# Optimization experiments

Hardware: AMD Instinct MI355X
Metric: run time of the kernel (lower is better)

## Reference

```python
import jax, jax.numpy as jnp
import numpy as np

CH = 64          # channels per plane
GS = 256         # base grid size
N_PTS = 500_000  # query points
BOUND = 1.0
A = -0.75        # torch bicubic coefficient


def _avg_pool(p):
    # torch F.avg_pool2d(kernel=3, stride=2, padding=1, count_include_pad=True) on (C,H,W)
    s = jax.lax.reduce_window(p, 0.0, jax.lax.add, (1, 3, 3), (1, 2, 2),
                              [(0, 0), (1, 1), (1, 1)])
    return s / 9.0


def _cubic_w(t):
    # Keys cubic conv weights (a=-0.75) for taps at offsets [-1,0,1,2]; t in [0,1). -> (4, M)
    def k1(x):  # |x| <= 1
        return ((A + 2.0) * x - (A + 3.0)) * x * x + 1.0
    def k2(x):  # 1 < |x| < 2
        return ((A * x - 5.0 * A) * x + 8.0 * A) * x - 4.0 * A
    return jnp.stack([k2(t + 1.0), k1(t), k1(1.0 - t), k2(2.0 - t)])


def _sample_plane(plane, gx, gy):
    # bicubic grid_sample, padding_mode='border', align_corners=True
    # plane: (C,H,W); gx,gy: (M,) grid coords in [-1,1] convention. -> (M,C)
    C, H, W = plane.shape
    x = (gx + 1.0) * 0.5 * (W - 1)  # unnormalize (align_corners=True)
    y = (gy + 1.0) * 0.5 * (H - 1)
    x0 = jnp.floor(x)
    y0 = jnp.floor(y)
    wx = _cubic_w(x - x0)  # (4,M)
    wy = _cubic_w(y - y0)  # (4,M)
    offs = jnp.arange(-1, 3, dtype=jnp.int32)[:, None]
    ix = jnp.clip(x0.astype(jnp.int32)[None, :] + offs, 0, W - 1)  # (4,M) border clamp
    iy = jnp.clip(y0.astype(jnp.int32)[None, :] + offs, 0, H - 1)
    out = jnp.zeros((C, x.shape[0]), plane.dtype)
    for j in range(4):
        row = wx[0] * plane[:, iy[j], ix[0]]
        for i in range(1, 4):
            row = row + wx[i] * plane[:, iy[j], ix[i]]  # (C,M) gather + fma
        out = out + wy[j] * row
    return out.T  # (M,C)


def setup_inputs() -> dict:
    key = jax.random.key(0)
    kc, kx, ky, kz = jax.random.split(key, 4)
    coordinates = jax.random.uniform(kc, (N_PTS, 3), jnp.float32, -1.0, 1.0)
    px0 = jax.random.normal(kx, (CH, GS, GS), jnp.float32) * 0.001
    py0 = jax.random.normal(ky, (CH, GS, GS), jnp.float32) * 0.001
    pz0 = jax.random.normal(kz, (CH, GS, GS), jnp.float32) * 0.001
    px1, py1, pz1 = _avg_pool(px0), _avg_pool(py0), _avg_pool(pz0)
    px2, py2, pz2 = _avg_pool(px1), _avg_pool(py1), _avg_pool(pz1)
    return dict(coordinates=coordinates, px0=px0, py0=py0, pz0=pz0,
                px1=px1, py1=py1, pz1=pz1, px2=px2, py2=py2, pz2=pz2)


def reference(coordinates, px0, py0, pz0, px1, py1, pz1, px2, py2, pz2):
    # Faithful to torch: coords mapped to [0,1] and fed to grid_sample as-is
    c = (coordinates + BOUND) / (2.0 * BOUND)  # (N,3), lives in [0,1] of the [-1,1] grid space
    feats = []
    for pxy, pyz, pxz in ((px0, py0, pz0), (px1, py1, pz1), (px2, py2, pz2)):
        f = (_sample_plane(pxy, c[:, 0], c[:, 1])
             + _sample_plane(pyz, c[:, 1], c[:, 2])
             + _sample_plane(pxz, c[:, 0], c[:, 2]))
        feats.append(f)
    return jnp.concatenate(feats, axis=-1)  # (N, 3*CH)
```

## Files before the change

kernel.cpp:

```cpp
#include <hip/hip_runtime.h>
#include <hip/hip_fp16.h>

#define NPTS 500000
#define NBINS 32768
#define NSUPER 8192

#define PLANE_SCALE 1024.0f
#define INV_PLANE_SCALE 0.0009765625f

__device__ __forceinline__ void cubic_w(float t, float w[4]) {
  const float a = -0.75f;
  const float t1 = t + 1.0f;
  w[0] = ((a * t1 - 5.0f * a) * t1 + 8.0f * a) * t1 - 4.0f * a;
  w[1] = ((a + 2.0f) * t - (a + 3.0f)) * t * t + 1.0f;
  const float u = 1.0f - t;
  w[2] = ((a + 2.0f) * u - (a + 3.0f)) * u * u + 1.0f;
  const float t2 = 2.0f - t;
  w[3] = ((a * t2 - 5.0f * a) * t2 + 8.0f * a) * t2 - 4.0f * a;
}

__global__ __launch_bounds__(256) void transpose_chw_hwc_f16(
    const float* __restrict__ p0, const float* __restrict__ p1,
    const float* __restrict__ p2, __half* __restrict__ dst, int HW) {
  __shared__ float lds[64][65];
  const float* src = (blockIdx.y == 0) ? p0 : ((blockIdx.y == 1) ? p1 : p2);
  __half* out = dst + (size_t)blockIdx.y * (size_t)HW * 64;
  const int pixBase = blockIdx.x * 64;
  const int tid = threadIdx.x;
  const int lane = tid & 63;
  const int quad = tid >> 6;
#pragma unroll
  for (int k = 0; k < 16; ++k) {
    const int c = k * 4 + quad;
    lds[c][lane] = src[(size_t)c * HW + pixBase + lane];
  }
  __syncthreads();
#pragma unroll
  for (int k = 0; k < 16; ++k) {
    const int pp = k * 4 + quad;
    out[(size_t)(pixBase + pp) * 64 + lane] =
        __float2half(lds[lane][pp] * PLANE_SCALE);
  }
}

__device__ __forceinline__ unsigned spread3(unsigned v) {
  return (v & 1u) | ((v & 2u) << 2) | ((v & 4u) << 4) | ((v & 8u) << 6) |
         ((v & 16u) << 8);
}

__device__ __forceinline__ unsigned compact3(unsigned v) {
  return (v & 1u) | ((v >> 2) & 2u) | ((v >> 4) & 4u) | ((v >> 6) & 8u) |
         ((v >> 8) & 16u);
}

__device__ __forceinline__ int bin_of(float cx, float cy, float cz) {
  int xq = (int)((cx + 1.0f) * 16.0f);
  int yq = (int)((cy + 1.0f) * 16.0f);
  int zq = (int)((cz + 1.0f) * 16.0f);
  xq = xq < 0 ? 0 : (xq > 31 ? 31 : xq);
  yq = yq < 0 ? 0 : (yq > 31 ? 31 : yq);
  zq = zq < 0 ? 0 : (zq > 31 ? 31 : zq);
  return (int)(spread3((unsigned)xq) | (spread3((unsigned)yq) << 1) |
               (spread3((unsigned)zq) << 2));
}

__global__ __launch_bounds__(256) void bin_count(
    const float* __restrict__ coords, int* __restrict__ counts) {
  const int pt = blockIdx.x * 256 + threadIdx.x;
  if (pt >= NPTS) return;
  const int b = bin_of(coords[pt * 3], coords[pt * 3 + 1], coords[pt * 3 + 2]);
  atomicAdd(&counts[b], 1);
}

__global__ __launch_bounds__(1024) void bin_scan(
    const int* __restrict__ counts, int* __restrict__ cursor) {
  __shared__ int lds[1024];
  const int t = threadIdx.x;
  const int base = t * 32;
  int s = 0;
#pragma unroll
  for (int i = 0; i < 32; ++i) s += counts[base + i];
  lds[t] = s;
  __syncthreads();
  int own = s;
  for (int off = 1; off < 1024; off <<= 1) {
    int v = (t >= off) ? lds[t - off] : 0;
    __syncthreads();
    lds[t] += v;
    __syncthreads();
  }
  int run = lds[t] - own;
#pragma unroll
  for (int i = 0; i < 32; ++i) {
    cursor[base + i] = run;
    run += counts[base + i];
  }
}

__global__ __launch_bounds__(256) void bin_scatter_prep(
    const float* __restrict__ coords, int* __restrict__ cursor,
    uint4* __restrict__ wrec) {
  const int pt = blockIdx.x * 256 + threadIdx.x;
  if (pt >= NPTS) return;
  const float x = coords[pt * 3], y = coords[pt * 3 + 1],
              z = coords[pt * 3 + 2];
  const int b = bin_of(x, y, z);
  const int pos = atomicAdd(&cursor[b], 1);

  const int qx0 = ((int)compact3((unsigned)b)) & ~1;
  const int qy0 = ((int)compact3((unsigned)b >> 1)) & ~1;
  const int qz = (int)compact3((unsigned)b >> 2);
  const float vin[3] = {x, y, z};

#pragma unroll
  for (int s = 0; s < 3; ++s) {
    const int W = (s == 0) ? 256 : ((s == 1) ? 128 : 64);
    const float hw = 0.5f * (float)(W - 1);
    const int fb[3] = {(int)floorf((1.0f + (float)qx0 * 0.03125f) * hw),
                       (int)floorf((1.0f + (float)qy0 * 0.03125f) * hw),
                       (int)floorf((1.0f + (float)qz * 0.03125f) * hw)};
    uint wp[6];
    int rel[3];
#pragma unroll
    for (int a = 0; a < 3; ++a) {
      const float c = (vin[a] + 1.0f) * 0.5f;
      const float gx = (c + 1.0f) * 0.5f * (float)(W - 1);
      const float x0f = floorf(gx);
      float w[4];
      cubic_w(gx - x0f, w);
      int r = (int)x0f - fb[a];
      const int rmax = (a == 2) ? 4 : 12;
      r = r < 0 ? 0 : (r > rmax ? rmax : r);
      rel[a] = r;
      const __half2 lo = __halves2half2(__float2half(w[0]), __float2half(w[1]));
      const __half2 hi = __halves2half2(__float2half(w[2]), __float2half(w[3]));
      wp[a * 2] = *(const uint*)&lo;
      wp[a * 2 + 1] = *(const uint*)&hi;
    }
    uint4* dst = wrec + ((size_t)s * NPTS + pos) * 2;
    dst[0] = make_uint4(wp[0], wp[1], wp[2], wp[3]);
    dst[1] = make_uint4(
        wp[4], wp[5],
        (uint)(rel[0] * 4) | ((uint)(rel[1] * 4) << 8) | ((uint)rel[2] << 16),
        (uint)pt);
  }
}

__global__ __launch_bounds__(256, 4) void sample_super(
    const uint4* __restrict__ wrec, const ushort* __restrict__ tp,
    const int* __restrict__ endc, float* __restrict__ out) {
  __shared__ uint4 win[2048];

  const int orig = blockIdx.x;
  const int sb = (orig & 7) * (NSUPER / 8) + (orig >> 3);
  const int b0 = sb * 4;
  const int start = (b0 == 0) ? 0 : endc[b0 - 1];
  const int end = endc[b0 + 3];
  if (start >= end) return;

  const int s = blockIdx.y;
  const int h = blockIdx.z;
  const int W = (s == 0) ? 256 : ((s == 1) ? 128 : 64);
  const size_t sbase = (s == 0) ? 0 : ((s == 1) ? 12582912 : 15728640);
  const size_t psz = (size_t)W * W * 64;
  const float hw = 0.5f * (float)(W - 1);

  const int qx0 = ((int)compact3((unsigned)b0)) & ~1;
  const int qy0 = ((int)compact3((unsigned)b0 >> 1)) & ~1;
  const int qz = (int)compact3((unsigned)b0 >> 2);
  const int wbx = (int)floorf((1.0f + (float)qx0 * 0.03125f) * hw) - 1;
  const int wby = (int)floorf((1.0f + (float)qy0 * 0.03125f) * hw) - 1;
  const int wbz = (int)floorf((1.0f + (float)qz * 0.03125f) * hw) - 1;

  const char* tpb = (const char*)(tp + sbase) + h * 64;
  const int tid = threadIdx.x;
  const int wave = tid >> 6;
  const int lane = tid & 63;
  const int px = lane >> 2;
  const int cgl = lane & 3;
#pragma unroll
  for (int k = 0; k < 8; ++k) {
    const int row = k * 4 + wave;
    int p, grow, cb;
    if (row < 16) {
      p = 0;
      grow = wby + row;
      cb = wbx;
    } else if (row < 24) {
      p = 1;
      grow = wbz + row - 16;
      cb = wby;
    } else {
      p = 2;
      grow = wbz + row - 24;
      cb = wbx;
    }
    grow = grow < 0 ? 0 : (grow > W - 1 ? W - 1 : grow);
    int gcol = cb + px;
    gcol = gcol < 0 ? 0 : (gcol > W - 1 ? W - 1 : gcol);
    const char* src = tpb + (size_t)p * psz * 2 +
                      ((size_t)grow * W + gcol) * 128 + cgl * 16;
#if __has_builtin(__builtin_amdgcn_global_load_lds)
    __builtin_amdgcn_global_load_lds((const uint*)src,
                                     (uint*)&win[row * 64], 16, 0, 0);
#else
    win[row * 64 + lane] = *reinterpret_cast<const uint4*>(src);
#endif
  }
  __syncthreads();

  const int lanegrp = tid >> 3;
  const int i8 = tid & 7;
  const int cg = tid & 3;
  const int colpair = (tid >> 2) & 1;

  for (int i0 = start; i0 < end; i0 += 32) {
    const int slot = i0 + lanegrp;
    if (slot >= end) break;
    const uint4 r0 = wrec[((size_t)s * NPTS + slot) * 2];
    const uint4 r1 = wrec[((size_t)s * NPTS + slot) * 2 + 1];
    const int pt = (int)r1.w;
    const int relx4 = (int)(r1.z & 255u);
    const int rely4 = (int)((r1.z >> 8) & 255u);
    const int relz = (int)((r1.z >> 16) & 255u);
    const int rely = rely4 >> 2;

    const __half2 hx01 = *(const __half2*)&r0.x;
    const __half2 hx23 = *(const __half2*)&r0.y;
    const __half2 hy01 = *(const __half2*)&r0.z;
    const __half2 hy23 = *(const __half2*)&r0.w;
    const __half2 hz01 = *(const __half2*)&r1.x;
    const __half2 hz23 = *(const __half2*)&r1.y;
    __half2 wyb[4], wzb[4];
    wyb[0] = __half2half2(__low2half(hy01));
    wyb[1] = __half2half2(__high2half(hy01));
    wyb[2] = __half2half2(__low2half(hy23));
    wyb[3] = __half2half2(__high2half(hy23));
    wzb[0] = __half2half2(__low2half(hz01));
    wzb[1] = __half2half2(__high2half(hz01));
    wzb[2] = __half2half2(__low2half(hz23));
    wzb[3] = __half2half2(__high2half(hz23));
    const __half2 cxA =
        __half2half2(colpair ? __high2half(hx01) : __low2half(hx01));
    const __half2 cxB =
        __half2half2(colpair ? __high2half(hx23) : __low2half(hx23));
    const __half2 cyA =
        __half2half2(colpair ? __high2half(hy01) : __low2half(hy01));
    const __half2 cyB =
        __half2half2(colpair ? __high2half(hy23) : __low2half(hy23));

    const int bXY = rely * 64 + relx4 + i8;
    const int bYZ = 1024 + relz * 64 + rely4 + i8;
    const int bXZ = 1536 + relz * 64 + relx4 + i8;

    __half2 acc0 = __float2half2_rn(0.0f), acc1 = acc0, acc2 = acc0,
            acc3 = acc0;

#define PLANE(BASE, CWA, CWB, RW)                                   \
  _Pragma("unroll") for (int j = 0; j < 4; ++j) {                   \
    const __half2 mA = __hmul2(CWA, RW[j]);                         \
    const __half2 mB = __hmul2(CWB, RW[j]);                         \
    const uint4 vA = win[(BASE) + j * 64];                          \
    const uint4 vB = win[(BASE) + j * 64 + 8];                      \
    acc0 = __hfma2(mA, *(const __half2*)&vA.x, acc0);               \
    acc1 = __hfma2(mA, *(const __half2*)&vA.y, acc1);               \
    acc2 = __hfma2(mA, *(const __half2*)&vA.z, acc2);               \
    acc3 = __hfma2(mA, *(const __half2*)&vA.w, acc3);               \
    acc0 = __hfma2(mB, *(const __half2*)&vB.x, acc0);               \
    acc1 = __hfma2(mB, *(const __half2*)&vB.y, acc1);               \
    acc2 = __hfma2(mB, *(const __half2*)&vB.z, acc2);               \
    acc3 = __hfma2(mB, *(const __half2*)&vB.w, acc3);               \
  }

    PLANE(bXY, cxA, cxB, wyb);
    PLANE(bYZ, cyA, cyB, wzb);
    PLANE(bXZ, cxA, cxB, wzb);
#undef PLANE

    {
      uint u0 = *(const uint*)&acc0, u1 = *(const uint*)&acc1,
           u2 = *(const uint*)&acc2, u3 = *(const uint*)&acc3;
      const uint p0 = __shfl_xor((int)u0, 4, 64);
      const uint p1 = __shfl_xor((int)u1, 4, 64);
      const uint p2 = __shfl_xor((int)u2, 4, 64);
      const uint p3 = __shfl_xor((int)u3, 4, 64);
      acc0 = __hadd2(acc0, *(const __half2*)&p0);
      acc1 = __hadd2(acc1, *(const __half2*)&p1);
      acc2 = __hadd2(acc2, *(const __half2*)&p2);
      acc3 = __hadd2(acc3, *(const __half2*)&p3);
    }

    const __half2 o0 = colpair ? acc2 : acc0;
    const __half2 o1 = colpair ? acc3 : acc1;
    const float2 f0 = __half22float2(o0);
    const float2 f1 = __half22float2(o1);
    *reinterpret_cast<float4*>(out + (size_t)pt * 192 + s * 64 + h * 32 +
                               cg * 8 + colpair * 4) =
        make_float4(f0.x * INV_PLANE_SCALE, f0.y * INV_PLANE_SCALE,
                    f1.x * INV_PLANE_SCALE, f1.y * INV_PLANE_SCALE);
  }
}

__device__ __forceinline__ void sample_acc_chw(const float* __restrict__ plane,
                                               int W, float gx, float gy,
                                               int cg, float4& acc) {
  const float x = (gx + 1.0f) * 0.5f * (float)(W - 1);
  const float y = (gy + 1.0f) * 0.5f * (float)(W - 1);
  const float x0f = floorf(x), y0f = floorf(y);
  float wx[4], wy[4];
  cubic_w(x - x0f, wx);
  cubic_w(y - y0f, wy);
  const int x0 = (int)x0f, y0 = (int)y0f;
  int ix[4], iy[4];
#pragma unroll
  for (int i = 0; i < 4; ++i) {
    int xi = x0 - 1 + i;
    ix[i] = xi < 0 ? 0 : (xi > W - 1 ? W - 1 : xi);
    int yi = y0 - 1 + i;
    iy[i] = yi < 0 ? 0 : (yi > W - 1 ? W - 1 : yi);
  }
  const size_t HW = (size_t)W * W;
  float r[4] = {acc.x, acc.y, acc.z, acc.w};
#pragma unroll
  for (int cc = 0; cc < 4; ++cc) {
    const float* pc = plane + (size_t)(cg * 4 + cc) * HW;
    float a = 0.f;
#pragma unroll
    for (int j = 0; j < 4; ++j) {
      const float* rb = pc + (size_t)iy[j] * W;
      float row = 0.f;
#pragma unroll
      for (int i = 0; i < 4; ++i) row += wx[i] * rb[ix[i]];
      a += wy[j] * row;
    }
    r[cc] += a;
  }
  acc = make_float4(r[0], r[1], r[2], r[3]);
}

__global__ __launch_bounds__(256) void sample_fallback(
    const float* __restrict__ coords, const float* __restrict__ px0,
    const float* __restrict__ py0, const float* __restrict__ pz0,
    const float* __restrict__ px1, const float* __restrict__ py1,
    const float* __restrict__ pz1, const float* __restrict__ px2,
    const float* __restrict__ py2, const float* __restrict__ pz2,
    float* __restrict__ out) {
  const int t = blockIdx.x * 256 + threadIdx.x;
  const int pt = t >> 4;
  const int cg = t & 15;
  if (pt >= NPTS) return;
  const float cx = (coords[pt * 3 + 0] + 1.0f) * 0.5f;
  const float cy = (coords[pt * 3 + 1] + 1.0f) * 0.5f;
  const float cz = (coords[pt * 3 + 2] + 1.0f) * 0.5f;
  const float* xs[3] = {px0, px1, px2};
  const float* ys[3] = {py0, py1, py2};
  const float* zs[3] = {pz0, pz1, pz2};
  const int sw[3] = {256, 128, 64};
  float* optr = out + (size_t)pt * 192 + cg * 4;
#pragma unroll
  for (int s = 0; s < 3; ++s) {
    const int W = sw[s];
    float4 acc = make_float4(0.f, 0.f, 0.f, 0.f);
    sample_acc_chw(xs[s], W, cx, cy, cg, acc);
    sample_acc_chw(ys[s], W, cy, cz, cg, acc);
    sample_acc_chw(zs[s], W, cx, cz, cg, acc);
    *reinterpret_cast<float4*>(optr + s * 64) = acc;
  }
}

extern "C" void kernel_launch(void* const* d_in, const int* in_sizes, int n_in,
                              void* d_out, int out_size, void* d_ws,
                              size_t ws_size, hipStream_t stream) {
  const float* coords = (const float*)d_in[0];
  const float* px0 = (const float*)d_in[1];
  const float* py0 = (const float*)d_in[2];
  const float* pz0 = (const float*)d_in[3];
  const float* px1 = (const float*)d_in[4];
  const float* py1 = (const float*)d_in[5];
  const float* pz1 = (const float*)d_in[6];
  const float* px2 = (const float*)d_in[7];
  const float* py2 = (const float*)d_in[8];
  const float* pz2 = (const float*)d_in[9];
  float* out = (float*)d_out;

  const size_t TP_BYTES = 33030144;
  const size_t CNT_OFF = TP_BYTES;
  const size_t CUR_OFF = CNT_OFF + 131072;
  const size_t REC_OFF = CUR_OFF + 131072;
  const size_t NEEDED = REC_OFF + (size_t)NPTS * 3 * 32;

  if (ws_size >= NEEDED) {
    __half* tp = (__half*)d_ws;
    int* counts = (int*)((char*)d_ws + CNT_OFF);
    int* cursor = (int*)((char*)d_ws + CUR_OFF);
    uint4* wrec = (uint4*)((char*)d_ws + REC_OFF);

    transpose_chw_hwc_f16<<<dim3(65536 / 64, 3), 256, 0, stream>>>(
        px0, py0, pz0, tp + 0, 65536);
    transpose_chw_hwc_f16<<<dim3(16384 / 64, 3), 256, 0, stream>>>(
        px1, py1, pz1, tp + 12582912, 16384);
    transpose_chw_hwc_f16<<<dim3(4096 / 64, 3), 256, 0, stream>>>(
        px2, py2, pz2, tp + 15728640, 4096);

    hipMemsetAsync(counts, 0, NBINS * sizeof(int), stream);
    const int pblocks = (NPTS + 255) / 256;
    bin_count<<<pblocks, 256, 0, stream>>>(coords, counts);
    bin_scan<<<1, 1024, 0, stream>>>(counts, cursor);
    bin_scatter_prep<<<pblocks, 256, 0, stream>>>(coords, cursor, wrec);

    sample_super<<<dim3(NSUPER, 3, 2), 256, 0, stream>>>(
        wrec, (const ushort*)tp, cursor, out);
  } else {
    const int sample_blocks = (NPTS * 16 + 255) / 256;
    sample_fallback<<<sample_blocks, 256, 0, stream>>>(
        coords, px0, py0, pz0, px1, py1, pz1, px2, py2, pz2, out);
  }
}
```

Baseline: 322.9 us.

## Use per-scale superbin sizes with a smaller LDS window

The superbin grouping now depends on scale. The finest scale groups 4 bins with a 12x16 window, and the coarser scales group 16 bins, so fewer blocks each reuse a loaded plane window over more points. The LDS window shrinks from 2048 to 1792 entries (rows 16/8/8 become 12/8/8), and launch bounds go from 4 to 5 blocks per CU to raise occupancy. The relative offsets and clamp limits in prep are changed to match the new window shapes. In exchange, the grid still launches 8192 blocks for every scale, and those beyond the superbin count for scales 1 and 2 exit immediately.

```diff
diff --git a/kernel.cpp b/kernel.cpp
--- a/kernel.cpp
+++ b/kernel.cpp
@@ -3,7 +3,6 @@
 
 #define NPTS 500000
 #define NBINS 32768
-#define NSUPER 8192
 
 #define PLANE_SCALE 1024.0f
 #define INV_PLANE_SCALE 0.0009765625f
@@ -107,18 +106,17 @@
   const int b = bin_of(x, y, z);
   const int pos = atomicAdd(&cursor[b], 1);
 
-  const int qx0 = ((int)compact3((unsigned)b)) & ~1;
-  const int qy0 = ((int)compact3((unsigned)b >> 1)) & ~1;
-  const int qz = (int)compact3((unsigned)b >> 2);
   const float vin[3] = {x, y, z};
 
 #pragma unroll
   for (int s = 0; s < 3; ++s) {
     const int W = (s == 0) ? 256 : ((s == 1) ? 128 : 64);
     const float hw = 0.5f * (float)(W - 1);
-    const int fb[3] = {(int)floorf((1.0f + (float)qx0 * 0.03125f) * hw),
-                       (int)floorf((1.0f + (float)qy0 * 0.03125f) * hw),
-                       (int)floorf((1.0f + (float)qz * 0.03125f) * hw)};
+    const int msk = (s == 0) ? 3 : 15;
+    const int bm = b & ~msk;
+    const int q0[3] = {(int)compact3((unsigned)bm),
+                       (int)compact3((unsigned)bm >> 1),
+                       (int)compact3((unsigned)bm >> 2)};
     uint wp[6];
     int rel[3];
 #pragma unroll
@@ -128,8 +126,9 @@
       const float x0f = floorf(gx);
       float w[4];
       cubic_w(gx - x0f, w);
-      int r = (int)x0f - fb[a];
-      const int rmax = (a == 2) ? 4 : 12;
+      const int fb = (int)floorf((1.0f + (float)q0[a] * 0.03125f) * hw);
+      int r = (int)x0f - fb;
+      const int rmax = (a == 0) ? 12 : ((a == 1) ? 8 : 4);
       r = r < 0 ? 0 : (r > rmax ? rmax : r);
       rel[a] = r;
       const __half2 lo = __halves2half2(__float2half(w[0]), __float2half(w[1]));
@@ -146,31 +145,34 @@
   }
 }
 
-__global__ __launch_bounds__(256, 4) void sample_super(
+__global__ __launch_bounds__(256, 5) void sample_super(
     const uint4* __restrict__ wrec, const ushort* __restrict__ tp,
     const int* __restrict__ endc, float* __restrict__ out) {
-  __shared__ uint4 win[2048];
-
+  __shared__ uint4 win[1792];
+
+  const int s = blockIdx.y;
+  const int NSUP = (s == 0) ? 8192 : 2048;
+  const int m = (s == 0) ? 4 : 16;
   const int orig = blockIdx.x;
-  const int sb = (orig & 7) * (NSUPER / 8) + (orig >> 3);
-  const int b0 = sb * 4;
+  if (orig >= NSUP) return;
+  const int sb = (orig & 7) * (NSUP / 8) + (orig >> 3);
+  const int b0 = sb * m;
   const int start = (b0 == 0) ? 0 : endc[b0 - 1];
-  const int end = endc[b0 + 3];
+  const int end = endc[b0 + m - 1];
   if (start >= end) return;
 
-  const int s = blockIdx.y;
   const int h = blockIdx.z;
   const int W = (s == 0) ? 256 : ((s == 1) ? 128 : 64);
   const size_t sbase = (s == 0) ? 0 : ((s == 1) ? 12582912 : 15728640);
   const size_t psz = (size_t)W * W * 64;
   const float hw = 0.5f * (float)(W - 1);
 
-  const int qx0 = ((int)compact3((unsigned)b0)) & ~1;
-  const int qy0 = ((int)compact3((unsigned)b0 >> 1)) & ~1;
-  const int qz = (int)compact3((unsigned)b0 >> 2);
+  const int qx0 = (int)compact3((unsigned)b0);
+  const int qy0 = (int)compact3((unsigned)b0 >> 1);
+  const int qz0 = (int)compact3((unsigned)b0 >> 2);
   const int wbx = (int)floorf((1.0f + (float)qx0 * 0.03125f) * hw) - 1;
   const int wby = (int)floorf((1.0f + (float)qy0 * 0.03125f) * hw) - 1;
-  const int wbz = (int)floorf((1.0f + (float)qz * 0.03125f) * hw) - 1;
+  const int wbz = (int)floorf((1.0f + (float)qz0 * 0.03125f) * hw) - 1;
 
   const char* tpb = (const char*)(tp + sbase) + h * 64;
   const int tid = threadIdx.x;
@@ -179,20 +181,20 @@
   const int px = lane >> 2;
   const int cgl = lane & 3;
 #pragma unroll
-  for (int k = 0; k < 8; ++k) {
+  for (int k = 0; k < 7; ++k) {
     const int row = k * 4 + wave;
     int p, grow, cb;
-    if (row < 16) {
+    if (row < 12) {
       p = 0;
       grow = wby + row;
       cb = wbx;
-    } else if (row < 24) {
+    } else if (row < 20) {
       p = 1;
-      grow = wbz + row - 16;
+      grow = wbz + row - 12;
       cb = wby;
     } else {
       p = 2;
-      grow = wbz + row - 24;
+      grow = wbz + row - 20;
       cb = wbx;
     }
     grow = grow < 0 ? 0 : (grow > W - 1 ? W - 1 : grow);
@@ -250,8 +252,8 @@
         __half2half2(colpair ? __high2half(hy23) : __low2half(hy23));
 
     const int bXY = rely * 64 + relx4 + i8;
-    const int bYZ = 1024 + relz * 64 + rely4 + i8;
-    const int bXZ = 1536 + relz * 64 + relx4 + i8;
+    const int bYZ = 768 + relz * 64 + rely4 + i8;
+    const int bXZ = 1280 + relz * 64 + relx4 + i8;
 
     __half2 acc0 = __float2half2_rn(0.0f), acc1 = acc0, acc2 = acc0,
             acc3 = acc0;
@@ -408,7 +410,7 @@
     bin_scan<<<1, 1024, 0, stream>>>(counts, cursor);
     bin_scatter_prep<<<pblocks, 256, 0, stream>>>(coords, cursor, wrec);
 
-    sample_super<<<dim3(NSUPER, 3, 2), 256, 0, stream>>>(
+    sample_super<<<dim3(8192, 3, 2), 256, 0, stream>>>(
         wrec, (const ushort*)tp, cursor, out);
   } else {
     const int sample_blocks = (NPTS * 16 + 255) / 256;
```

Measured after the change: 285.0 us. 1.13x faster.
